# Optimization experiments

Measured on AMD Instinct MI355X. Metric: run time of the kernel, lower is better.

## Reference

```python
import jax, jax.numpy as jnp
import numpy as np

TAU = 0.5        # init kwarg tau
NUM_SEG = 1024   # int(sp_seg.max()) + 1; fixed for jit (randint upper bound)
EPS = 1e-8       # torch F.cosine_similarity eps


def _cos(a, b):
    # cosine similarity along last axis, torch-style eps clamping of norms
    dot = jnp.sum(a * b, axis=-1)
    na = jnp.maximum(jnp.linalg.norm(a, axis=-1), EPS)
    nb = jnp.maximum(jnp.linalg.norm(b, axis=-1), EPS)
    return dot / (na * nb)


def setup_inputs() -> dict:
    key = jax.random.key(0)
    k1, k2, k3 = jax.random.split(key, 3)
    embeddings = jax.random.normal(k1, (1, 32, 1024, 1024), dtype=jnp.float32)
    sp_seg = jax.random.randint(k2, (1, 1, 1024, 1024), 0, NUM_SEG, dtype=jnp.int32)
    edges = jax.random.randint(k3, (2, 8192), 0, NUM_SEG, dtype=jnp.int32)
    return {"embeddings": embeddings, "sp_seg": sp_seg, "edges": edges}


def reference(embeddings, sp_seg, edges):
    C = embeddings.shape[1]
    emb = embeddings.reshape(C, -1).T            # (N, C), N = H*W
    seg = sp_seg.reshape(-1)                     # (N,) segment id per pixel
    # segment means (replaces the dense one-hot scatter mask of the original)
    sums = jax.ops.segment_sum(emb, seg, num_segments=NUM_SEG)      # (S, C)
    counts = jax.ops.segment_sum(jnp.ones_like(seg, dtype=emb.dtype), seg,
                                 num_segments=NUM_SEG)              # (S,)
    means = sums / jnp.maximum(counts, 1.0)[:, None]                # (S, C)
    # intra: cos(mean of pixel's segment, pixel embedding) -- one value per pixel
    intra = _cos(means[seg], emb) / TAU          # (N,)
    # inter: cos between segment means of each RAG edge
    inter = _cos(means[edges[0]], means[edges[1]]) / TAU            # (E,)
    denom = jnp.sum(jnp.exp(intra)) + jnp.sum(jnp.exp(inter))       # scalar
    # -log(exp(intra)/denom) = log(denom) - intra, averaged over pixels
    return jnp.mean(jnp.log(denom) - intra)
```

## Files before the change

kernel.cpp:

```cpp
#include <hip/hip_runtime.h>
#include <math.h>

#define N_PIX (1024 * 1024)
#define NSEG 1024
#define NCH 32
#define NCHUNK 16
#define NEDGE 8192
#define EPS 1e-8f
#define INV_TAU 2.0f
#define SCALE 262144.0f
#define INV_SCALE (1.0f / 262144.0f)

#define OFF_GSUMI 0
#define OFF_GCNTI (OFF_GSUMI + NCHUNK * NCH * NSEG)
#define OFF_MEANSN (OFF_GCNTI + NCHUNK * 16 * NSEG)
#define OFF_BPE (OFF_MEANSN + NSEG * NCH)
#define OFF_BPI (OFF_BPE + 512)
#define OFF_IPE (OFF_BPI + 512)

__global__ __launch_bounds__(1024) void k_segsum(const float* __restrict__ emb,
                                                 const int* __restrict__ seg,
                                                 int* __restrict__ gsum_i,
                                                 int* __restrict__ gcnt_i) {
    __shared__ int lsum[NSEG];
    __shared__ int lcnt[NSEG];
    const int bid = blockIdx.x;
    const int c = bid >> 4;
    const int j = bid & 15;
    const int t = threadIdx.x;

    lsum[t] = 0;
    lcnt[t] = 0;
    __syncthreads();

    const int chunk = N_PIX / NCHUNK;
    const float* ec = emb + (size_t)c * N_PIX + (size_t)j * chunk;
    const int* sg = seg + j * chunk;

    for (int it = 0; it < chunk / (1024 * 4); ++it) {
        const int idx = (it * 1024 + t) * 4;
        const float4 v = *(const float4*)(ec + idx);
        const int4 s4 = *(const int4*)(sg + idx);
        atomicAdd(&lsum[s4.x], __float2int_rn(v.x * SCALE));
        atomicAdd(&lsum[s4.y], __float2int_rn(v.y * SCALE));
        atomicAdd(&lsum[s4.z], __float2int_rn(v.z * SCALE));
        atomicAdd(&lsum[s4.w], __float2int_rn(v.w * SCALE));
        if (it == c) {
            atomicAdd(&lcnt[s4.x], 1);
            atomicAdd(&lcnt[s4.y], 1);
            atomicAdd(&lcnt[s4.z], 1);
            atomicAdd(&lcnt[s4.w], 1);
        }
    }
    __syncthreads();

    gsum_i[(j * NCH + c) * NSEG + t] = lsum[t];
    if (c < 16) gcnt_i[(j * 16 + c) * NSEG + t] = lcnt[t];
}

__global__ void k_means(const int* __restrict__ gsum_i,
                        const int* __restrict__ gcnt_i,
                        float* __restrict__ meansn) {
    const int s = blockIdx.x * 256 + threadIdx.x;
    int cnt_i = 0;
#pragma unroll 16
    for (int p = 0; p < NCHUNK * 16; ++p) cnt_i += gcnt_i[p * NSEG + s];
    const float inv = 1.0f / fmaxf((float)cnt_i, 1.0f);
    float m[NCH];
    float nrm = 0.0f;
#pragma unroll
    for (int c = 0; c < NCH; ++c) {
        int a = 0;
#pragma unroll
        for (int j = 0; j < NCHUNK; ++j) a += gsum_i[(j * NCH + c) * NSEG + s];
        m[c] = (float)a * INV_SCALE * inv;
        nrm += m[c] * m[c];
    }
    const float rn = 1.0f / fmaxf(sqrtf(nrm), EPS);
#pragma unroll
    for (int c = 0; c < NCH; ++c) meansn[s * NCH + c] = m[c] * rn;
}

__global__ __launch_bounds__(512) void k_intra(const float* __restrict__ emb,
                                               const int* __restrict__ seg,
                                               const float* __restrict__ meansn,
                                               float* __restrict__ bpe,
                                               float* __restrict__ bpi) {
    const int g = blockIdx.x * 512 + threadIdx.x;
    const int n0 = g * 4;
    const int4 s4 = *(const int4*)(seg + n0);

    float dot0 = 0.f, dot1 = 0.f, dot2 = 0.f, dot3 = 0.f;
    float nr0 = 0.f, nr1 = 0.f, nr2 = 0.f, nr3 = 0.f;

#pragma unroll
    for (int c0 = 0; c0 < NCH; c0 += 4) {
        const float4 e0 = *(const float4*)(emb + (size_t)(c0 + 0) * N_PIX + n0);
        const float4 e1 = *(const float4*)(emb + (size_t)(c0 + 1) * N_PIX + n0);
        const float4 e2 = *(const float4*)(emb + (size_t)(c0 + 2) * N_PIX + n0);
        const float4 e3 = *(const float4*)(emb + (size_t)(c0 + 3) * N_PIX + n0);
        const float4 m0 = *(const float4*)(meansn + s4.x * NCH + c0);
        const float4 m1 = *(const float4*)(meansn + s4.y * NCH + c0);
        const float4 m2 = *(const float4*)(meansn + s4.z * NCH + c0);
        const float4 m3 = *(const float4*)(meansn + s4.w * NCH + c0);

        dot0 += m0.x * e0.x + m0.y * e1.x + m0.z * e2.x + m0.w * e3.x;
        dot1 += m1.x * e0.y + m1.y * e1.y + m1.z * e2.y + m1.w * e3.y;
        dot2 += m2.x * e0.z + m2.y * e1.z + m2.z * e2.z + m2.w * e3.z;
        dot3 += m3.x * e0.w + m3.y * e1.w + m3.z * e2.w + m3.w * e3.w;

        nr0 += e0.x * e0.x + e1.x * e1.x + e2.x * e2.x + e3.x * e3.x;
        nr1 += e0.y * e0.y + e1.y * e1.y + e2.y * e2.y + e3.y * e3.y;
        nr2 += e0.z * e0.z + e1.z * e1.z + e2.z * e2.z + e3.z * e3.z;
        nr3 += e0.w * e0.w + e1.w * e1.w + e2.w * e2.w + e3.w * e3.w;
    }

    const float i0 = dot0 / fmaxf(sqrtf(nr0), EPS) * INV_TAU;
    const float i1 = dot1 / fmaxf(sqrtf(nr1), EPS) * INV_TAU;
    const float i2 = dot2 / fmaxf(sqrtf(nr2), EPS) * INV_TAU;
    const float i3 = dot3 / fmaxf(sqrtf(nr3), EPS) * INV_TAU;
    float esum = expf(i0) + expf(i1) + expf(i2) + expf(i3);
    float isum = i0 + i1 + i2 + i3;

#pragma unroll
    for (int off = 32; off > 0; off >>= 1) {
        esum += __shfl_down(esum, off);
        isum += __shfl_down(isum, off);
    }
    __shared__ float we[8], wi[8];
    const int wid = threadIdx.x >> 6;
    const int lane = threadIdx.x & 63;
    if (lane == 0) { we[wid] = esum; wi[wid] = isum; }
    __syncthreads();
    if (threadIdx.x == 0) {
        float a = 0.f, b = 0.f;
#pragma unroll
        for (int w = 0; w < 8; ++w) { a += we[w]; b += wi[w]; }
        bpe[blockIdx.x] = a;
        bpi[blockIdx.x] = b;
    }
}

__global__ void k_inter(const int* __restrict__ edges,
                        const float* __restrict__ meansn,
                        float* __restrict__ ipe) {
    const int e = blockIdx.x * 256 + threadIdx.x;
    const int a = edges[e];
    const int b = edges[NEDGE + e];
    float dot = 0.0f;
#pragma unroll
    for (int c0 = 0; c0 < NCH; c0 += 4) {
        const float4 ma = *(const float4*)(meansn + a * NCH + c0);
        const float4 mb = *(const float4*)(meansn + b * NCH + c0);
        dot += ma.x * mb.x + ma.y * mb.y + ma.z * mb.z + ma.w * mb.w;
    }
    float ex = expf(dot * INV_TAU);
#pragma unroll
    for (int off = 32; off > 0; off >>= 1) ex += __shfl_down(ex, off);
    __shared__ float we[4];
    const int wid = threadIdx.x >> 6;
    const int lane = threadIdx.x & 63;
    if (lane == 0) we[wid] = ex;
    __syncthreads();
    if (threadIdx.x == 0) ipe[blockIdx.x] = we[0] + we[1] + we[2] + we[3];
}

__global__ void k_final(const float* __restrict__ bpe,
                        const float* __restrict__ bpi,
                        const float* __restrict__ ipe,
                        float* __restrict__ out) {
    const int t = threadIdx.x;
    float e = bpe[t] + (t < 32 ? ipe[t] : 0.0f);
    float i = bpi[t];
#pragma unroll
    for (int off = 32; off > 0; off >>= 1) {
        e += __shfl_down(e, off);
        i += __shfl_down(i, off);
    }
    __shared__ float we[8], wi[8];
    const int wid = t >> 6;
    const int lane = t & 63;
    if (lane == 0) { we[wid] = e; wi[wid] = i; }
    __syncthreads();
    if (t == 0) {
        float E = 0.f, I = 0.f;
#pragma unroll
        for (int w = 0; w < 8; ++w) { E += we[w]; I += wi[w]; }
        out[0] = logf(E) - I * (1.0f / (float)N_PIX);
    }
}

extern "C" void kernel_launch(void* const* d_in, const int* in_sizes, int n_in,
                              void* d_out, int out_size, void* d_ws, size_t ws_size,
                              hipStream_t stream) {
    (void)in_sizes; (void)n_in; (void)out_size; (void)ws_size;
    const float* emb = (const float*)d_in[0];
    const int* seg = (const int*)d_in[1];
    const int* edges = (const int*)d_in[2];
    float* out = (float*)d_out;

    int* wsi = (int*)d_ws;
    float* wsf = (float*)d_ws;
    int* gsum_i = wsi + OFF_GSUMI;
    int* gcnt_i = wsi + OFF_GCNTI;
    float* meansn = wsf + OFF_MEANSN;
    float* bpe = wsf + OFF_BPE;
    float* bpi = wsf + OFF_BPI;
    float* ipe = wsf + OFF_IPE;

    k_segsum<<<512, 1024, 0, stream>>>(emb, seg, gsum_i, gcnt_i);
    k_means<<<4, 256, 0, stream>>>(gsum_i, gcnt_i, meansn);
    k_intra<<<512, 512, 0, stream>>>(emb, seg, meansn, bpe, bpi);
    k_inter<<<NEDGE / 256, 256, 0, stream>>>(edges, meansn, ipe);
    k_final<<<1, 512, 0, stream>>>(bpe, bpi, ipe, out);
}
```

Before: 263.6 us.

## Fuse all stages into one cooperative kernel with grid-wide syncs

Merges the five launches (segment sum, means, intra, inter, final) into a single cooperative kernel of 256 blocks of 1024 threads, separated by grid.sync barriers, so launch gaps between stages disappear. The segment-sum stage now splits pixels into 8 chunks instead of 16, and the means stage is spread across all blocks with wave shuffles instead of running on 4 small blocks. The trade-off is a grid of only 256 blocks for the bandwidth-heavy phases, plus the cost of the grid barriers.

```diff
diff --git a/kernel.cpp b/kernel.cpp
--- a/kernel.cpp
+++ b/kernel.cpp
@@ -1,10 +1,13 @@
 #include <hip/hip_runtime.h>
+#include <hip/hip_cooperative_groups.h>
 #include <math.h>
+
+namespace cg = cooperative_groups;
 
 #define N_PIX (1024 * 1024)
 #define NSEG 1024
 #define NCH 32
-#define NCHUNK 16
+#define NCHUNK 8
 #define NEDGE 8192
 #define EPS 1e-8f
 #define INV_TAU 2.0f
@@ -13,180 +16,183 @@
 
 #define OFF_GSUMI 0
 #define OFF_GCNTI (OFF_GSUMI + NCHUNK * NCH * NSEG)
-#define OFF_MEANSN (OFF_GCNTI + NCHUNK * 16 * NSEG)
+#define OFF_MEANSN (OFF_GCNTI + NCHUNK * NCH * NSEG)
 #define OFF_BPE (OFF_MEANSN + NSEG * NCH)
-#define OFF_BPI (OFF_BPE + 512)
-#define OFF_IPE (OFF_BPI + 512)
-
-__global__ __launch_bounds__(1024) void k_segsum(const float* __restrict__ emb,
-                                                 const int* __restrict__ seg,
-                                                 int* __restrict__ gsum_i,
-                                                 int* __restrict__ gcnt_i) {
+#define OFF_BPI (OFF_BPE + 256)
+#define OFF_IPE (OFF_BPI + 256)
+
+__global__ __launch_bounds__(1024) void k_fused(const float* __restrict__ emb,
+                                                const int* __restrict__ seg,
+                                                const int* __restrict__ edges,
+                                                int* __restrict__ gsum_i,
+                                                int* __restrict__ gcnt_i,
+                                                float* __restrict__ meansn,
+                                                float* __restrict__ bpe,
+                                                float* __restrict__ bpi,
+                                                float* __restrict__ ipe,
+                                                float* __restrict__ out) {
+    cg::grid_group grid = cg::this_grid();
     __shared__ int lsum[NSEG];
     __shared__ int lcnt[NSEG];
+    __shared__ float we[16], wi[16];
     const int bid = blockIdx.x;
-    const int c = bid >> 4;
-    const int j = bid & 15;
     const int t = threadIdx.x;
 
-    lsum[t] = 0;
-    lcnt[t] = 0;
-    __syncthreads();
-
-    const int chunk = N_PIX / NCHUNK;
-    const float* ec = emb + (size_t)c * N_PIX + (size_t)j * chunk;
-    const int* sg = seg + j * chunk;
-
-    for (int it = 0; it < chunk / (1024 * 4); ++it) {
-        const int idx = (it * 1024 + t) * 4;
-        const float4 v = *(const float4*)(ec + idx);
-        const int4 s4 = *(const int4*)(sg + idx);
-        atomicAdd(&lsum[s4.x], __float2int_rn(v.x * SCALE));
-        atomicAdd(&lsum[s4.y], __float2int_rn(v.y * SCALE));
-        atomicAdd(&lsum[s4.z], __float2int_rn(v.z * SCALE));
-        atomicAdd(&lsum[s4.w], __float2int_rn(v.w * SCALE));
-        if (it == c) {
-            atomicAdd(&lcnt[s4.x], 1);
-            atomicAdd(&lcnt[s4.y], 1);
-            atomicAdd(&lcnt[s4.z], 1);
-            atomicAdd(&lcnt[s4.w], 1);
-        }
-    }
-    __syncthreads();
-
-    gsum_i[(j * NCH + c) * NSEG + t] = lsum[t];
-    if (c < 16) gcnt_i[(j * 16 + c) * NSEG + t] = lcnt[t];
-}
-
-__global__ void k_means(const int* __restrict__ gsum_i,
-                        const int* __restrict__ gcnt_i,
-                        float* __restrict__ meansn) {
-    const int s = blockIdx.x * 256 + threadIdx.x;
-    int cnt_i = 0;
-#pragma unroll 16
-    for (int p = 0; p < NCHUNK * 16; ++p) cnt_i += gcnt_i[p * NSEG + s];
-    const float inv = 1.0f / fmaxf((float)cnt_i, 1.0f);
-    float m[NCH];
-    float nrm = 0.0f;
-#pragma unroll
-    for (int c = 0; c < NCH; ++c) {
-        int a = 0;
-#pragma unroll
-        for (int j = 0; j < NCHUNK; ++j) a += gsum_i[(j * NCH + c) * NSEG + s];
-        m[c] = (float)a * INV_SCALE * inv;
-        nrm += m[c] * m[c];
-    }
-    const float rn = 1.0f / fmaxf(sqrtf(nrm), EPS);
-#pragma unroll
-    for (int c = 0; c < NCH; ++c) meansn[s * NCH + c] = m[c] * rn;
-}
-
-__global__ __launch_bounds__(512) void k_intra(const float* __restrict__ emb,
-                                               const int* __restrict__ seg,
-                                               const float* __restrict__ meansn,
-                                               float* __restrict__ bpe,
-                                               float* __restrict__ bpi) {
-    const int g = blockIdx.x * 512 + threadIdx.x;
-    const int n0 = g * 4;
-    const int4 s4 = *(const int4*)(seg + n0);
-
-    float dot0 = 0.f, dot1 = 0.f, dot2 = 0.f, dot3 = 0.f;
-    float nr0 = 0.f, nr1 = 0.f, nr2 = 0.f, nr3 = 0.f;
-
-#pragma unroll
-    for (int c0 = 0; c0 < NCH; c0 += 4) {
-        const float4 e0 = *(const float4*)(emb + (size_t)(c0 + 0) * N_PIX + n0);
-        const float4 e1 = *(const float4*)(emb + (size_t)(c0 + 1) * N_PIX + n0);
-        const float4 e2 = *(const float4*)(emb + (size_t)(c0 + 2) * N_PIX + n0);
-        const float4 e3 = *(const float4*)(emb + (size_t)(c0 + 3) * N_PIX + n0);
-        const float4 m0 = *(const float4*)(meansn + s4.x * NCH + c0);
-        const float4 m1 = *(const float4*)(meansn + s4.y * NCH + c0);
-        const float4 m2 = *(const float4*)(meansn + s4.z * NCH + c0);
-        const float4 m3 = *(const float4*)(meansn + s4.w * NCH + c0);
-
-        dot0 += m0.x * e0.x + m0.y * e1.x + m0.z * e2.x + m0.w * e3.x;
-        dot1 += m1.x * e0.y + m1.y * e1.y + m1.z * e2.y + m1.w * e3.y;
-        dot2 += m2.x * e0.z + m2.y * e1.z + m2.z * e2.z + m2.w * e3.z;
-        dot3 += m3.x * e0.w + m3.y * e1.w + m3.z * e2.w + m3.w * e3.w;
-
-        nr0 += e0.x * e0.x + e1.x * e1.x + e2.x * e2.x + e3.x * e3.x;
-        nr1 += e0.y * e0.y + e1.y * e1.y + e2.y * e2.y + e3.y * e3.y;
-        nr2 += e0.z * e0.z + e1.z * e1.z + e2.z * e2.z + e3.z * e3.z;
-        nr3 += e0.w * e0.w + e1.w * e1.w + e2.w * e2.w + e3.w * e3.w;
-    }
-
-    const float i0 = dot0 / fmaxf(sqrtf(nr0), EPS) * INV_TAU;
-    const float i1 = dot1 / fmaxf(sqrtf(nr1), EPS) * INV_TAU;
-    const float i2 = dot2 / fmaxf(sqrtf(nr2), EPS) * INV_TAU;
-    const float i3 = dot3 / fmaxf(sqrtf(nr3), EPS) * INV_TAU;
-    float esum = expf(i0) + expf(i1) + expf(i2) + expf(i3);
-    float isum = i0 + i1 + i2 + i3;
-
-#pragma unroll
-    for (int off = 32; off > 0; off >>= 1) {
-        esum += __shfl_down(esum, off);
-        isum += __shfl_down(isum, off);
-    }
-    __shared__ float we[8], wi[8];
-    const int wid = threadIdx.x >> 6;
-    const int lane = threadIdx.x & 63;
-    if (lane == 0) { we[wid] = esum; wi[wid] = isum; }
-    __syncthreads();
-    if (threadIdx.x == 0) {
-        float a = 0.f, b = 0.f;
-#pragma unroll
-        for (int w = 0; w < 8; ++w) { a += we[w]; b += wi[w]; }
-        bpe[blockIdx.x] = a;
-        bpi[blockIdx.x] = b;
-    }
-}
-
-__global__ void k_inter(const int* __restrict__ edges,
-                        const float* __restrict__ meansn,
-                        float* __restrict__ ipe) {
-    const int e = blockIdx.x * 256 + threadIdx.x;
-    const int a = edges[e];
-    const int b = edges[NEDGE + e];
-    float dot = 0.0f;
-#pragma unroll
-    for (int c0 = 0; c0 < NCH; c0 += 4) {
-        const float4 ma = *(const float4*)(meansn + a * NCH + c0);
-        const float4 mb = *(const float4*)(meansn + b * NCH + c0);
-        dot += ma.x * mb.x + ma.y * mb.y + ma.z * mb.z + ma.w * mb.w;
-    }
-    float ex = expf(dot * INV_TAU);
-#pragma unroll
-    for (int off = 32; off > 0; off >>= 1) ex += __shfl_down(ex, off);
-    __shared__ float we[4];
-    const int wid = threadIdx.x >> 6;
-    const int lane = threadIdx.x & 63;
-    if (lane == 0) we[wid] = ex;
-    __syncthreads();
-    if (threadIdx.x == 0) ipe[blockIdx.x] = we[0] + we[1] + we[2] + we[3];
-}
-
-__global__ void k_final(const float* __restrict__ bpe,
-                        const float* __restrict__ bpi,
-                        const float* __restrict__ ipe,
-                        float* __restrict__ out) {
-    const int t = threadIdx.x;
-    float e = bpe[t] + (t < 32 ? ipe[t] : 0.0f);
-    float i = bpi[t];
-#pragma unroll
-    for (int off = 32; off > 0; off >>= 1) {
-        e += __shfl_down(e, off);
-        i += __shfl_down(i, off);
-    }
-    __shared__ float we[8], wi[8];
-    const int wid = t >> 6;
-    const int lane = t & 63;
-    if (lane == 0) { we[wid] = e; wi[wid] = i; }
-    __syncthreads();
-    if (t == 0) {
-        float E = 0.f, I = 0.f;
-#pragma unroll
-        for (int w = 0; w < 8; ++w) { E += we[w]; I += wi[w]; }
-        out[0] = logf(E) - I * (1.0f / (float)N_PIX);
+    {
+        const int c = bid >> 3;
+        const int j = bid & 7;
+        lsum[t] = 0;
+        lcnt[t] = 0;
+        __syncthreads();
+
+        const int chunk = N_PIX / NCHUNK;
+        const float* ec = emb + (size_t)c * N_PIX + (size_t)j * chunk;
+        const int* sg = seg + j * chunk;
+
+        for (int it = 0; it < chunk / (1024 * 4); ++it) {
+            const int idx = (it * 1024 + t) * 4;
+            const float4 v = *(const float4*)(ec + idx);
+            const int4 s4 = *(const int4*)(sg + idx);
+            atomicAdd(&lsum[s4.x], __float2int_rn(v.x * SCALE));
+            atomicAdd(&lsum[s4.y], __float2int_rn(v.y * SCALE));
+            atomicAdd(&lsum[s4.z], __float2int_rn(v.z * SCALE));
+            atomicAdd(&lsum[s4.w], __float2int_rn(v.w * SCALE));
+            if (it == c) {
+                atomicAdd(&lcnt[s4.x], 1);
+                atomicAdd(&lcnt[s4.y], 1);
+                atomicAdd(&lcnt[s4.z], 1);
+                atomicAdd(&lcnt[s4.w], 1);
+            }
+        }
+        __syncthreads();
+        gsum_i[(j * NCH + c) * NSEG + t] = lsum[t];
+        gcnt_i[(j * NCH + c) * NSEG + t] = lcnt[t];
+    }
+    grid.sync();
+
+    if (t < 128) {
+        const int sl = t >> 5;
+        const int cc = t & 31;
+        const int s = bid * 4 + sl;
+        int cn = 0, a = 0;
+#pragma unroll
+        for (int jj = 0; jj < NCHUNK; ++jj) {
+            cn += gcnt_i[(jj * NCH + cc) * NSEG + s];
+            a += gsum_i[(jj * NCH + cc) * NSEG + s];
+        }
+#pragma unroll
+        for (int m = 1; m < 32; m <<= 1) cn += __shfl_xor(cn, m);
+        const float mval = (float)a * INV_SCALE / fmaxf((float)cn, 1.0f);
+        float nm = mval * mval;
+#pragma unroll
+        for (int m = 1; m < 32; m <<= 1) nm += __shfl_xor(nm, m);
+        const float rn = 1.0f / fmaxf(sqrtf(nm), EPS);
+        meansn[bid * 128 + t] = mval * rn;
+    }
+    grid.sync();
+
+    {
+        const int n0 = (bid * 1024 + t) * 4;
+        const int4 s4 = *(const int4*)(seg + n0);
+
+        float dot0 = 0.f, dot1 = 0.f, dot2 = 0.f, dot3 = 0.f;
+        float nr0 = 0.f, nr1 = 0.f, nr2 = 0.f, nr3 = 0.f;
+
+#pragma unroll
+        for (int c0 = 0; c0 < NCH; c0 += 4) {
+            const float4 e0 = *(const float4*)(emb + (size_t)(c0 + 0) * N_PIX + n0);
+            const float4 e1 = *(const float4*)(emb + (size_t)(c0 + 1) * N_PIX + n0);
+            const float4 e2 = *(const float4*)(emb + (size_t)(c0 + 2) * N_PIX + n0);
+            const float4 e3 = *(const float4*)(emb + (size_t)(c0 + 3) * N_PIX + n0);
+            const float4 m0 = *(const float4*)(meansn + s4.x * NCH + c0);
+            const float4 m1 = *(const float4*)(meansn + s4.y * NCH + c0);
+            const float4 m2 = *(const float4*)(meansn + s4.z * NCH + c0);
+            const float4 m3 = *(const float4*)(meansn + s4.w * NCH + c0);
+
+            dot0 += m0.x * e0.x + m0.y * e1.x + m0.z * e2.x + m0.w * e3.x;
+            dot1 += m1.x * e0.y + m1.y * e1.y + m1.z * e2.y + m1.w * e3.y;
+            dot2 += m2.x * e0.z + m2.y * e1.z + m2.z * e2.z + m2.w * e3.z;
+            dot3 += m3.x * e0.w + m3.y * e1.w + m3.z * e2.w + m3.w * e3.w;
+
+            nr0 += e0.x * e0.x + e1.x * e1.x + e2.x * e2.x + e3.x * e3.x;
+            nr1 += e0.y * e0.y + e1.y * e1.y + e2.y * e2.y + e3.y * e3.y;
+            nr2 += e0.z * e0.z + e1.z * e1.z + e2.z * e2.z + e3.z * e3.z;
+            nr3 += e0.w * e0.w + e1.w * e1.w + e2.w * e2.w + e3.w * e3.w;
+        }
+
+        const float i0 = dot0 / fmaxf(sqrtf(nr0), EPS) * INV_TAU;
+        const float i1 = dot1 / fmaxf(sqrtf(nr1), EPS) * INV_TAU;
+        const float i2 = dot2 / fmaxf(sqrtf(nr2), EPS) * INV_TAU;
+        const float i3 = dot3 / fmaxf(sqrtf(nr3), EPS) * INV_TAU;
+        float esum = expf(i0) + expf(i1) + expf(i2) + expf(i3);
+        float isum = i0 + i1 + i2 + i3;
+
+#pragma unroll
+        for (int off = 32; off > 0; off >>= 1) {
+            esum += __shfl_down(esum, off);
+            isum += __shfl_down(isum, off);
+        }
+        const int wid = t >> 6;
+        const int lane = t & 63;
+        if (lane == 0) { we[wid] = esum; wi[wid] = isum; }
+        __syncthreads();
+        if (t == 0) {
+            float a = 0.f, b = 0.f;
+#pragma unroll
+            for (int w = 0; w < 16; ++w) { a += we[w]; b += wi[w]; }
+            bpe[bid] = a;
+            bpi[bid] = b;
+        }
+        __syncthreads();
+    }
+
+    if (bid < 8) {
+        const int e = bid * 1024 + t;
+        const int a = edges[e];
+        const int b = edges[NEDGE + e];
+        float dot = 0.0f;
+#pragma unroll
+        for (int c0 = 0; c0 < NCH; c0 += 4) {
+            const float4 ma = *(const float4*)(meansn + a * NCH + c0);
+            const float4 mb = *(const float4*)(meansn + b * NCH + c0);
+            dot += ma.x * mb.x + ma.y * mb.y + ma.z * mb.z + ma.w * mb.w;
+        }
+        float ex = expf(dot * INV_TAU);
+#pragma unroll
+        for (int off = 32; off > 0; off >>= 1) ex += __shfl_down(ex, off);
+        const int wid = t >> 6;
+        const int lane = t & 63;
+        if (lane == 0) we[wid] = ex;
+        __syncthreads();
+        if (t == 0) {
+            float a2 = 0.f;
+#pragma unroll
+            for (int w = 0; w < 16; ++w) a2 += we[w];
+            ipe[bid] = a2;
+        }
+    }
+    grid.sync();
+
+    if (bid == 0) {
+        float ev = (t < 256) ? bpe[t] : 0.0f;
+        float iv = (t < 256) ? bpi[t] : 0.0f;
+        if (t < 8) ev += ipe[t];
+#pragma unroll
+        for (int off = 32; off > 0; off >>= 1) {
+            ev += __shfl_down(ev, off);
+            iv += __shfl_down(iv, off);
+        }
+        const int wid = t >> 6;
+        const int lane = t & 63;
+        __syncthreads();
+        if (lane == 0) { we[wid] = ev; wi[wid] = iv; }
+        __syncthreads();
+        if (t == 0) {
+            float E = 0.f, I = 0.f;
+#pragma unroll
+            for (int w = 0; w < 16; ++w) { E += we[w]; I += wi[w]; }
+            out[0] = logf(E) - I * (1.0f / (float)N_PIX);
+        }
     }
 }
 
@@ -208,9 +214,8 @@
     float* bpi = wsf + OFF_BPI;
     float* ipe = wsf + OFF_IPE;
 
-    k_segsum<<<512, 1024, 0, stream>>>(emb, seg, gsum_i, gcnt_i);
-    k_means<<<4, 256, 0, stream>>>(gsum_i, gcnt_i, meansn);
-    k_intra<<<512, 512, 0, stream>>>(emb, seg, meansn, bpe, bpi);
-    k_inter<<<NEDGE / 256, 256, 0, stream>>>(edges, meansn, ipe);
-    k_final<<<1, 512, 0, stream>>>(bpe, bpi, ipe, out);
+    void* args[] = {&emb, &seg, &edges, &gsum_i, &gcnt_i,
+                    &meansn, &bpe, &bpi, &ipe, &out};
+    hipLaunchCooperativeKernel((const void*)k_fused, dim3(256), dim3(1024),
+                               args, 0, stream);
 }
```

Measured after the change: 345.6 us. 1.31x slower.
